# Optimization experiments

Measured on AMD Instinct MI355X. Metric: run time of the kernel, lower is better.

Reference implementation:

```python
import jax, jax.numpy as jnp
import numpy as np

B, N, C = 4, 2048, 1024
H = 8
D = C // H  # head dim = 128
SCALE = D ** -0.5
EPS = 1e-5


def setup_inputs() -> dict:
    key = jax.random.key(0)
    ks = jax.random.split(key, 12)
    s = 0.02
    return {
        "x": jax.random.normal(ks[0], (B, N, C), jnp.float32),
        "ln1_g": jnp.ones((C,), jnp.float32),
        "ln1_b": jnp.zeros((C,), jnp.float32),
        "w_qkv": jax.random.normal(ks[1], (3 * C, C), jnp.float32) * s,  # torch Linear weight [out,in], no bias
        "w_proj": jax.random.normal(ks[2], (C, C), jnp.float32) * s,
        "b_proj": jnp.zeros((C,), jnp.float32),
        "ln2_g": jnp.ones((C,), jnp.float32),
        "ln2_b": jnp.zeros((C,), jnp.float32),
        "w1": jax.random.normal(ks[3], (C, C), jnp.float32) * s,
        "b1": jnp.full((C,), 0.1, jnp.float32),
        "w2": jax.random.normal(ks[4], (C, C), jnp.float32) * s,
        "b2": jnp.full((C,), 0.1, jnp.float32),
        "bn_g": jnp.ones((C,), jnp.float32),
        "bn_b": jnp.zeros((C,), jnp.float32),
        "bn_mean": jnp.zeros((C,), jnp.float32),
        "bn_var": jnp.ones((C,), jnp.float32),
    }


def _layernorm(x, g, b):
    mu = jnp.mean(x, axis=-1, keepdims=True)
    var = jnp.mean(jnp.square(x - mu), axis=-1, keepdims=True)
    return (x - mu) * jax.lax.rsqrt(var + EPS) * g + b


def reference(x, ln1_g, ln1_b, w_qkv, w_proj, b_proj, ln2_g, ln2_b,
              w1, b1, w2, b2, bn_g, bn_b, bn_mean, bn_var):
    # --- attention branch (pre-LN) ---
    h = _layernorm(x, ln1_g, ln1_b)
    qkv = h @ w_qkv.T                              # [B,N,3C]
    qkv = qkv.reshape(B, N, 3, H, D)
    q = qkv[:, :, 0].transpose(0, 2, 1, 3)         # [B,H,N,D]
    k = qkv[:, :, 1].transpose(0, 2, 1, 3)
    v = qkv[:, :, 2].transpose(0, 2, 1, 3)
    attn = jnp.einsum('bhnd,bhmd->bhnm', q, k) * SCALE
    attn = jax.nn.softmax(attn, axis=-1)
    o = jnp.einsum('bhnm,bhmd->bhnd', attn, v)     # [B,H,N,D]
    o = o.transpose(0, 2, 1, 3).reshape(B, N, C)
    x = x + (o @ w_proj.T + b_proj)

    # --- MLP branch (pre-LN), ELU + eval-mode BatchNorm ---
    h = _layernorm(x, ln2_g, ln2_b)
    h = jax.nn.elu(h @ w1.T + b1)
    h = jax.nn.elu(h @ w2.T + b2)
    h = (h - bn_mean) * jax.lax.rsqrt(bn_var + EPS) * bn_g + bn_b
    return x + h
```

## Files before the change

kernel.cpp:

```cpp
#include <hip/hip_runtime.h>
#include <hip/hip_bf16.h>

using u16 = unsigned short;
typedef __attribute__((ext_vector_type(8))) __bf16 bf16x8;
typedef __attribute__((ext_vector_type(4))) float f32x4;
typedef __attribute__((ext_vector_type(16))) float f32x16;
typedef __attribute__((ext_vector_type(4))) unsigned int u32x4;

#define LN_EPS 1e-5f
#define ATT_SCALE 0.08838834764831845f

__device__ __forceinline__ u16 f2bf(float f) {
    unsigned int u = __builtin_bit_cast(unsigned int, f);
    u += 0x7FFFu + ((u >> 16) & 1u);
    return (u16)(u >> 16);
}

__device__ __forceinline__ bf16x8 ld_frag(const u16* p) {
    return __builtin_bit_cast(bf16x8, *(const u32x4*)p);
}

__device__ __forceinline__ unsigned pack_bf2(float lo, float hi) {
    return __builtin_amdgcn_perm(__builtin_bit_cast(unsigned, hi),
                                 __builtin_bit_cast(unsigned, lo), 0x07060302u);
}

__global__ void cvt_f32_bf16(const float* __restrict__ in, u16* __restrict__ out, int n4) {
    int i = blockIdx.x * blockDim.x + threadIdx.x;
    if (i < n4) {
        const float4 v = ((const float4*)in)[i];
        ushort4 o;
        o.x = f2bf(v.x); o.y = f2bf(v.y); o.z = f2bf(v.z); o.w = f2bf(v.w);
        ((ushort4*)out)[i] = o;
    }
}

__global__ __launch_bounds__(256)
void ln_kernel(const float* __restrict__ x, const float* __restrict__ g,
               const float* __restrict__ b, u16* __restrict__ out)
{
    const int row = blockIdx.x;
    const int t = threadIdx.x;
    const float4 v = ((const float4*)(x + (size_t)row * 1024))[t];
    float s  = v.x + v.y + v.z + v.w;
    float ss = v.x * v.x + v.y * v.y + v.z * v.z + v.w * v.w;
    #pragma unroll
    for (int d = 32; d > 0; d >>= 1) { s += __shfl_down(s, d); ss += __shfl_down(ss, d); }
    __shared__ float red[8];
    const int wave = t >> 6, lane = t & 63;
    if (lane == 0) { red[wave] = s; red[4 + wave] = ss; }
    __syncthreads();
    const float S  = red[0] + red[1] + red[2] + red[3];
    const float SS = red[4] + red[5] + red[6] + red[7];
    const float mu = S * (1.f / 1024.f);
    const float rstd = rsqrtf(SS * (1.f / 1024.f) - mu * mu + LN_EPS);
    const float4 gv = ((const float4*)g)[t];
    const float4 bv = ((const float4*)b)[t];
    ushort4 ov;
    ov.x = f2bf((v.x - mu) * rstd * gv.x + bv.x);
    ov.y = f2bf((v.y - mu) * rstd * gv.y + bv.y);
    ov.z = f2bf((v.z - mu) * rstd * gv.z + bv.z);
    ov.w = f2bf((v.w - mu) * rstd * gv.w + bv.w);
    ((ushort4*)(out + (size_t)row * 1024))[t] = ov;
}

template <int EPI>
__global__ __launch_bounds__(256, 2)
void gemm_bt(const u16* __restrict__ A, const u16* __restrict__ Bw,
             int M, int N, int K,
             const float* __restrict__ bias, const float* __restrict__ res,
             float* __restrict__ Cf, u16* __restrict__ Cb, u16* __restrict__ Cv,
             const float* __restrict__ bng, const float* __restrict__ bnb,
             const float* __restrict__ bnm, const float* __restrict__ bnv)
{
    __shared__ __align__(16) u16 As[128 * 32];
    __shared__ __align__(16) u16 Bs[128 * 32];

    const int tid  = threadIdx.x;
    const int wave = tid >> 6;
    const int lane = tid & 63;
    const int quad = lane >> 4;
    const int l16  = lane & 15;
    const int m0 = blockIdx.x * 128;
    const int n0 = blockIdx.y * 128;
    const int wm = (wave & 1) * 64;
    const int wn = (wave >> 1) * 64;

    f32x4 acc[4][4];
    #pragma unroll
    for (int i = 0; i < 4; i++)
        #pragma unroll
        for (int j = 0; j < 4; j++)
            acc[i][j] = f32x4{0.f, 0.f, 0.f, 0.f};

    const int srow = lane >> 2;
    const int scol = (lane & 3) * 8;
    const u16* gA0 = A  + (size_t)(m0 + wave * 32 + srow) * K + scol;
    const u16* gA1 = gA0 + (size_t)16 * K;
    const u16* gB0 = Bw + (size_t)(n0 + wave * 32 + srow) * K + scol;
    const u16* gB1 = gB0 + (size_t)16 * K;
    u16* lA0 = &As[(wave * 32) * 32];
    u16* lA1 = &As[(wave * 32 + 16) * 32];
    u16* lB0 = &Bs[(wave * 32) * 32];
    u16* lB1 = &Bs[(wave * 32 + 16) * 32];

    for (int k0 = 0; k0 < K; k0 += 32) {
        __builtin_amdgcn_global_load_lds((const __attribute__((address_space(1))) void*)(gA0 + k0),
                                         (__attribute__((address_space(3))) void*)lA0, 16, 0, 0);
        __builtin_amdgcn_global_load_lds((const __attribute__((address_space(1))) void*)(gA1 + k0),
                                         (__attribute__((address_space(3))) void*)lA1, 16, 0, 0);
        __builtin_amdgcn_global_load_lds((const __attribute__((address_space(1))) void*)(gB0 + k0),
                                         (__attribute__((address_space(3))) void*)lB0, 16, 0, 0);
        __builtin_amdgcn_global_load_lds((const __attribute__((address_space(1))) void*)(gB1 + k0),
                                         (__attribute__((address_space(3))) void*)lB1, 16, 0, 0);
        __syncthreads();
        bf16x8 af[4], bfv[4];
        #pragma unroll
        for (int i = 0; i < 4; i++) af[i]  = ld_frag(&As[(wm + i * 16 + l16) * 32 + quad * 8]);
        #pragma unroll
        for (int j = 0; j < 4; j++) bfv[j] = ld_frag(&Bs[(wn + j * 16 + l16) * 32 + quad * 8]);
        #pragma unroll
        for (int i = 0; i < 4; i++)
            #pragma unroll
            for (int j = 0; j < 4; j++)
                acc[i][j] = __builtin_amdgcn_mfma_f32_16x16x32_bf16(af[i], bfv[j], acc[i][j], 0, 0, 0);
        __syncthreads();
    }

    #pragma unroll
    for (int j = 0; j < 4; j++) {
        const int gn = n0 + wn + j * 16 + l16;
        float bs = 0.f, sc = 0.f, sh = 0.f;
        if constexpr (EPI >= 1) bs = bias[gn];
        if constexpr (EPI == 3) {
            const float iv = rsqrtf(bnv[gn] + LN_EPS);
            sc = bng[gn] * iv;
            sh = bnb[gn] - bnm[gn] * sc;
        }
        if constexpr (EPI == 0) {
            if (gn < 2048) {
                const float qs = (gn < 1024) ? ATT_SCALE : 1.0f;
                #pragma unroll
                for (int i = 0; i < 4; i++) {
                    const int gm0 = m0 + wm + i * 16 + quad * 4;
                    #pragma unroll
                    for (int r = 0; r < 4; r++)
                        Cb[(size_t)(gm0 + r) * 2048 + gn] = f2bf(acc[i][j][r] * qs);
                }
            } else {
                const int hh = (gn >> 7) & 7, dd = gn & 127;
                #pragma unroll
                for (int i = 0; i < 4; i++) {
                    const int gm0 = m0 + wm + i * 16 + quad * 4;
                    #pragma unroll
                    for (int r = 0; r < 4; r++) {
                        const int tok = gm0 + r;
                        Cv[((size_t)((tok >> 11) * 8 + hh) * 128 + dd) * 2048 + (tok & 2047)] =
                            f2bf(acc[i][j][r]);
                    }
                }
            }
        } else {
            #pragma unroll
            for (int i = 0; i < 4; i++) {
                const int gm0 = m0 + wm + i * 16 + quad * 4;
                #pragma unroll
                for (int r = 0; r < 4; r++) {
                    const size_t idx = (size_t)(gm0 + r) * N + gn;
                    const float v = acc[i][j][r];
                    if constexpr (EPI == 1) {
                        Cf[idx] = res[idx] + v + bs;
                    } else if constexpr (EPI == 2) {
                        float t = v + bs;
                        t = t > 0.f ? t : (__expf(t) - 1.f);
                        Cb[idx] = f2bf(t);
                    } else {
                        float t = v + bs;
                        t = t > 0.f ? t : (__expf(t) - 1.f);
                        t = t * sc + sh;
                        Cf[idx] = res[idx] + t;
                    }
                }
            }
        }
    }
}

__global__ __launch_bounds__(256, 2)
void attn_kernel(const u16* __restrict__ qk, const u16* __restrict__ vT, u16* __restrict__ o)
{
    __shared__ __align__(16) u16 smem[17408];

    const int tid  = threadIdx.x;
    const int wave = tid >> 6;
    const int lane = tid & 63;
    const int l32  = lane & 31;
    const int hl   = lane >> 5;
    const int qt   = blockIdx.x;
    const int bh   = blockIdx.y;
    const int b    = bh >> 3, h = bh & 7;
    const size_t tok0 = (size_t)b * 2048;

    const u16* qptr = qk + h * 128;
    const u16* kptr = qk + 1024 + h * 128;
    const u16* vptr = vT + (size_t)bh * 128 * 2048;

    #pragma unroll
    for (int qq = 0; qq < 8; qq++) {
        const int s = qq * 256 + tid;
        const int r = s >> 4;
        const int cg = (s & 15) ^ (r & 7);
        const u16* g = qptr + (tok0 + qt * 128 + r) * 2048 + cg * 8;
        const int sb = (qq * 256 + (tid & 192)) * 8;
        __builtin_amdgcn_global_load_lds((const __attribute__((address_space(1))) void*)g,
                                         (__attribute__((address_space(3))) void*)(smem + sb), 16, 0, 0);
    }
    __syncthreads();

    bf16x8 qf[8];
    {
        const int row = wave * 32 + l32;
        #pragma unroll
        for (int ks = 0; ks < 8; ks++) {
            const int c = (ks * 2 + hl) ^ (row & 7);
            qf[ks] = ld_frag(smem + row * 128 + c * 8);
        }
    }

    f32x16 oacc[4];
    #pragma unroll
    for (int i = 0; i < 4; i++)
        #pragma unroll
        for (int e = 0; e < 16; e++) oacc[i][e] = 0.f;
    float l_acc = 0.f;

    u16* Ks = smem;
    u16* Vs = smem + 8192;

    for (int kt = 0; kt < 32; kt++) {
        __syncthreads();
        #pragma unroll
        for (int qq = 0; qq < 4; qq++) {
            const int s = qq * 256 + tid;
            const int r = s >> 4;
            const int cg = (s & 15) ^ (r & 7);
            const u16* g = kptr + (tok0 + kt * 64 + r) * 2048 + cg * 8;
            const int sb = (qq * 256 + (tid & 192)) * 8;
            __builtin_amdgcn_global_load_lds((const __attribute__((address_space(1))) void*)g,
                                             (__attribute__((address_space(3))) void*)(Ks + sb), 16, 0, 0);
        }
        #pragma unroll
        for (int qq = 0; qq < 4; qq++) {
            const int s = qq * 256 + tid;
            const int r = s >> 3;
            const int cg = (s & 7) ^ (r & 7);
            const u16* g = vptr + (size_t)r * 2048 + kt * 64 + cg * 8;
            const int sb = (qq * 256 + (tid & 192)) * 8;
            __builtin_amdgcn_global_load_lds((const __attribute__((address_space(1))) void*)g,
                                             (__attribute__((address_space(3))) void*)(Vs + sb), 16, 0, 0);
        }
        __syncthreads();

        f32x16 sacc[2];
        #pragma unroll
        for (int t = 0; t < 2; t++)
            #pragma unroll
            for (int e = 0; e < 16; e++) sacc[t][e] = 0.f;
        #pragma unroll
        for (int ks = 0; ks < 8; ks++) {
            #pragma unroll
            for (int mt = 0; mt < 2; mt++) {
                const int row = mt * 32 + l32;
                const int c = (ks * 2 + hl) ^ (row & 7);
                const bf16x8 kf = ld_frag(Ks + row * 128 + c * 8);
                sacc[mt] = __builtin_amdgcn_mfma_f32_32x32x16_bf16(kf, qf[ks], sacc[mt], 0, 0, 0);
            }
        }

        unsigned pk[2][8];
        #pragma unroll
        for (int t = 0; t < 2; t++) {
            #pragma unroll
            for (int r2 = 0; r2 < 8; r2++) {
                const float p0 = __expf(sacc[t][2 * r2]);
                const float p1 = __expf(sacc[t][2 * r2 + 1]);
                l_acc += p0 + p1;
                pk[t][r2] = pack_bf2(p0, p1);
            }
        }

        #pragma unroll
        for (int ks = 0; ks < 4; ks++) {
            const int t = ks >> 1;
            const int pb = (ks & 1) * 4;
            const unsigned s0 = (unsigned)__shfl_xor((int)pk[t][pb + 0], 32);
            const unsigned s1 = (unsigned)__shfl_xor((int)pk[t][pb + 1], 32);
            const unsigned s2 = (unsigned)__shfl_xor((int)pk[t][pb + 2], 32);
            const unsigned s3 = (unsigned)__shfl_xor((int)pk[t][pb + 3], 32);
            u32x4 pu;
            pu.x = hl ? s2 : pk[t][pb + 0];
            pu.y = hl ? s3 : pk[t][pb + 1];
            pu.z = hl ? pk[t][pb + 2] : s0;
            pu.w = hl ? pk[t][pb + 3] : s1;
            const bf16x8 pf = __builtin_bit_cast(bf16x8, pu);
            #pragma unroll
            for (int dt = 0; dt < 4; dt++) {
                const int row = dt * 32 + l32;
                const int c = (ks * 2 + hl) ^ (row & 7);
                const bf16x8 vf = ld_frag(Vs + row * 64 + c * 8);
                oacc[dt] = __builtin_amdgcn_mfma_f32_32x32x16_bf16(vf, pf, oacc[dt], 0, 0, 0);
            }
        }
    }

    __syncthreads();
    u16* Ot = smem;
    const float lt  = l_acc + __shfl_xor(l_acc, 32);
    const float inv = 1.0f / lt;
    const int qloc = wave * 32 + l32;
    #pragma unroll
    for (int dt = 0; dt < 4; dt++) {
        #pragma unroll
        for (int r2 = 0; r2 < 8; r2++) {
            const float v0 = oacc[dt][2 * r2] * inv;
            const float v1 = oacc[dt][2 * r2 + 1] * inv;
            const int dp = dt * 32 + 4 * hl + 2 * (r2 & 1) + 8 * (r2 >> 1);
            *(unsigned*)(Ot + qloc * 136 + dp) = pack_bf2(v0, v1);
        }
    }
    __syncthreads();
    const int qr = tid >> 1;
    const int hh = tid & 1;
    const u16* src = Ot + qr * 136 + hh * 64;
    u16* dst = o + (tok0 + qt * 128 + qr) * 1024 + h * 128 + hh * 64;
    #pragma unroll
    for (int c = 0; c < 8; c++)
        *(u32x4*)(dst + c * 8) = *(const u32x4*)(src + c * 8);
}

extern "C" void kernel_launch(void* const* d_in, const int* in_sizes, int n_in,
                              void* d_out, int out_size, void* d_ws, size_t ws_size,
                              hipStream_t stream)
{
    const float* x      = (const float*)d_in[0];
    const float* ln1_g  = (const float*)d_in[1];
    const float* ln1_b  = (const float*)d_in[2];
    const float* w_qkv  = (const float*)d_in[3];
    const float* w_proj = (const float*)d_in[4];
    const float* b_proj = (const float*)d_in[5];
    const float* ln2_g  = (const float*)d_in[6];
    const float* ln2_b  = (const float*)d_in[7];
    const float* w1     = (const float*)d_in[8];
    const float* b1     = (const float*)d_in[9];
    const float* w2     = (const float*)d_in[10];
    const float* b2     = (const float*)d_in[11];
    const float* bn_g   = (const float*)d_in[12];
    const float* bn_b   = (const float*)d_in[13];
    const float* bn_m   = (const float*)d_in[14];
    const float* bn_v   = (const float*)d_in[15];
    float* out = (float*)d_out;

    u16* wq   = (u16*)d_ws;
    u16* wp   = wq  + (size_t)3072 * 1024;
    u16* w1b  = wp  + (size_t)1024 * 1024;
    u16* w2b  = w1b + (size_t)1024 * 1024;
    u16* hbuf = w2b + (size_t)1024 * 1024;
    u16* qkb  = hbuf + (size_t)8192 * 1024;
    u16* vTb  = qkb + (size_t)8192 * 2048;
    u16* obuf = vTb + (size_t)8192 * 1024;
    float* x1 = (float*)(obuf + (size_t)8192 * 1024);

    cvt_f32_bf16<<<3072, 256, 0, stream>>>(w_qkv,  wq,  3072 * 1024 / 4);
    cvt_f32_bf16<<<1024, 256, 0, stream>>>(w_proj, wp,  1024 * 1024 / 4);
    cvt_f32_bf16<<<1024, 256, 0, stream>>>(w1,     w1b, 1024 * 1024 / 4);
    cvt_f32_bf16<<<1024, 256, 0, stream>>>(w2,     w2b, 1024 * 1024 / 4);

    ln_kernel<<<8192, 256, 0, stream>>>(x, ln1_g, ln1_b, hbuf);

    gemm_bt<0><<<dim3(64, 24), 256, 0, stream>>>(hbuf, wq, 8192, 3072, 1024,
        nullptr, nullptr, nullptr, qkb, vTb, nullptr, nullptr, nullptr, nullptr);

    attn_kernel<<<dim3(16, 32), 256, 0, stream>>>(qkb, vTb, obuf);

    gemm_bt<1><<<dim3(64, 8), 256, 0, stream>>>(obuf, wp, 8192, 1024, 1024,
        b_proj, x, x1, nullptr, nullptr, nullptr, nullptr, nullptr, nullptr);

    ln_kernel<<<8192, 256, 0, stream>>>(x1, ln2_g, ln2_b, hbuf);

    gemm_bt<2><<<dim3(64, 8), 256, 0, stream>>>(hbuf, w1b, 8192, 1024, 1024,
        b1, nullptr, nullptr, obuf, nullptr, nullptr, nullptr, nullptr, nullptr);

    gemm_bt<3><<<dim3(64, 8), 256, 0, stream>>>(obuf, w2b, 8192, 1024, 1024,
        b2, x1, out, nullptr, nullptr, bn_g, bn_b, bn_m, bn_v);
}
```

Measured before the change: 396.2 us.

## Double-buffer K/V tiles in attention, remap blocks, and use smaller GEMM tiles for C-wide GEMMs

The attention kernel now double-buffers its K/V tiles in shared memory, prefetching the next tile while the current one is computed, and drops one barrier per iteration. Blocks are remapped with a 1D grid so that neighbouring blocks share heads, which should help L2 reuse. The three 1024-wide GEMMs move to a new 64x128 tile kernel with a higher occupancy hint, which doubles the block count for better CU fill. In exchange, attention uses more LDS (64KB), which may reduce occupancy, and the smaller GEMM tiles reuse each loaded tile less.

Measured after the change: 400.4 us. About the same (+1.1%).

```diff
diff --git a/kernel.cpp b/kernel.cpp
--- a/kernel.cpp
+++ b/kernel.cpp
@@ -23,6 +23,11 @@
 __device__ __forceinline__ unsigned pack_bf2(float lo, float hi) {
     return __builtin_amdgcn_perm(__builtin_bit_cast(unsigned, hi),
                                  __builtin_bit_cast(unsigned, lo), 0x07060302u);
+}
+
+__device__ __forceinline__ void gl_lds(const u16* g, u16* l) {
+    __builtin_amdgcn_global_load_lds((const __attribute__((address_space(1))) void*)g,
+                                     (__attribute__((address_space(3))) void*)l, 16, 0, 0);
 }
 
 __global__ void cvt_f32_bf16(const float* __restrict__ in, u16* __restrict__ out, int n4) {
@@ -64,15 +69,11 @@
     ((ushort4*)(out + (size_t)row * 1024))[t] = ov;
 }
 
-template <int EPI>
 __global__ __launch_bounds__(256, 2)
-void gemm_bt(const u16* __restrict__ A, const u16* __restrict__ Bw,
-             int M, int N, int K,
-             const float* __restrict__ bias, const float* __restrict__ res,
-             float* __restrict__ Cf, u16* __restrict__ Cb, u16* __restrict__ Cv,
-             const float* __restrict__ bng, const float* __restrict__ bnb,
-             const float* __restrict__ bnm, const float* __restrict__ bnv)
+void gemm_qkv(const u16* __restrict__ A, const u16* __restrict__ Bw,
+              u16* __restrict__ Cb, u16* __restrict__ Cv)
 {
+    const int M = 8192, N = 3072, K = 1024;
     __shared__ __align__(16) u16 As[128 * 32];
     __shared__ __align__(16) u16 Bs[128 * 32];
 
@@ -105,14 +106,10 @@
     u16* lB1 = &Bs[(wave * 32 + 16) * 32];
 
     for (int k0 = 0; k0 < K; k0 += 32) {
-        __builtin_amdgcn_global_load_lds((const __attribute__((address_space(1))) void*)(gA0 + k0),
-                                         (__attribute__((address_space(3))) void*)lA0, 16, 0, 0);
-        __builtin_amdgcn_global_load_lds((const __attribute__((address_space(1))) void*)(gA1 + k0),
-                                         (__attribute__((address_space(3))) void*)lA1, 16, 0, 0);
-        __builtin_amdgcn_global_load_lds((const __attribute__((address_space(1))) void*)(gB0 + k0),
-                                         (__attribute__((address_space(3))) void*)lB0, 16, 0, 0);
-        __builtin_amdgcn_global_load_lds((const __attribute__((address_space(1))) void*)(gB1 + k0),
-                                         (__attribute__((address_space(3))) void*)lB1, 16, 0, 0);
+        gl_lds(gA0 + k0, lA0);
+        gl_lds(gA1 + k0, lA1);
+        gl_lds(gB0 + k0, lB0);
+        gl_lds(gB1 + k0, lB1);
         __syncthreads();
         bf16x8 af[4], bfv[4];
         #pragma unroll
@@ -130,56 +127,114 @@
     #pragma unroll
     for (int j = 0; j < 4; j++) {
         const int gn = n0 + wn + j * 16 + l16;
-        float bs = 0.f, sc = 0.f, sh = 0.f;
-        if constexpr (EPI >= 1) bs = bias[gn];
+        if (gn < 2048) {
+            const float qs = (gn < 1024) ? ATT_SCALE : 1.0f;
+            #pragma unroll
+            for (int i = 0; i < 4; i++) {
+                const int gm0 = m0 + wm + i * 16 + quad * 4;
+                #pragma unroll
+                for (int r = 0; r < 4; r++)
+                    Cb[(size_t)(gm0 + r) * 2048 + gn] = f2bf(acc[i][j][r] * qs);
+            }
+        } else {
+            const int hh = (gn >> 7) & 7, dd = gn & 127;
+            #pragma unroll
+            for (int i = 0; i < 4; i++) {
+                const int gm0 = m0 + wm + i * 16 + quad * 4;
+                #pragma unroll
+                for (int r = 0; r < 4; r++) {
+                    const int tok = gm0 + r;
+                    Cv[((size_t)((tok >> 11) * 8 + hh) * 128 + dd) * 2048 + (tok & 2047)] =
+                        f2bf(acc[i][j][r]);
+                }
+            }
+        }
+    }
+}
+
+template <int EPI>
+__global__ __launch_bounds__(256, 4)
+void gemm_c(const u16* __restrict__ A, const u16* __restrict__ Bw,
+            const float* __restrict__ bias, const float* __restrict__ res,
+            float* __restrict__ Cf, u16* __restrict__ Cb,
+            const float* __restrict__ bng, const float* __restrict__ bnb,
+            const float* __restrict__ bnm, const float* __restrict__ bnv)
+{
+    const int N = 1024, K = 1024;
+    __shared__ __align__(16) u16 As[64 * 32];
+    __shared__ __align__(16) u16 Bs[128 * 32];
+
+    const int tid  = threadIdx.x;
+    const int wave = tid >> 6;
+    const int lane = tid & 63;
+    const int quad = lane >> 4;
+    const int l16  = lane & 15;
+    const int m0 = blockIdx.x * 64;
+    const int n0 = blockIdx.y * 128;
+    const int wm = (wave & 1) * 32;
+    const int wn = (wave >> 1) * 64;
+
+    f32x4 acc[2][4];
+    #pragma unroll
+    for (int i = 0; i < 2; i++)
+        #pragma unroll
+        for (int j = 0; j < 4; j++)
+            acc[i][j] = f32x4{0.f, 0.f, 0.f, 0.f};
+
+    const int srow = tid >> 2;
+    const int scol = (tid & 3) * 8;
+    const u16* gA  = A  + (size_t)(m0 + srow) * K + scol;
+    const u16* gB0 = Bw + (size_t)(n0 + srow) * K + scol;
+    const u16* gB1 = gB0 + (size_t)64 * K;
+    u16* lA  = &As[wave * 512];
+    u16* lB0 = &Bs[wave * 512];
+    u16* lB1 = &Bs[2048 + wave * 512];
+
+    for (int k0 = 0; k0 < K; k0 += 32) {
+        gl_lds(gA  + k0, lA);
+        gl_lds(gB0 + k0, lB0);
+        gl_lds(gB1 + k0, lB1);
+        __syncthreads();
+        bf16x8 af[2], bfv[4];
+        #pragma unroll
+        for (int i = 0; i < 2; i++) af[i]  = ld_frag(&As[(wm + i * 16 + l16) * 32 + quad * 8]);
+        #pragma unroll
+        for (int j = 0; j < 4; j++) bfv[j] = ld_frag(&Bs[(wn + j * 16 + l16) * 32 + quad * 8]);
+        #pragma unroll
+        for (int i = 0; i < 2; i++)
+            #pragma unroll
+            for (int j = 0; j < 4; j++)
+                acc[i][j] = __builtin_amdgcn_mfma_f32_16x16x32_bf16(af[i], bfv[j], acc[i][j], 0, 0, 0);
+        __syncthreads();
+    }
+
+    #pragma unroll
+    for (int j = 0; j < 4; j++) {
+        const int gn = n0 + wn + j * 16 + l16;
+        float bs = bias[gn], sc = 0.f, sh = 0.f;
         if constexpr (EPI == 3) {
             const float iv = rsqrtf(bnv[gn] + LN_EPS);
             sc = bng[gn] * iv;
             sh = bnb[gn] - bnm[gn] * sc;
         }
-        if constexpr (EPI == 0) {
-            if (gn < 2048) {
-                const float qs = (gn < 1024) ? ATT_SCALE : 1.0f;
-                #pragma unroll
-                for (int i = 0; i < 4; i++) {
-                    const int gm0 = m0 + wm + i * 16 + quad * 4;
-                    #pragma unroll
-                    for (int r = 0; r < 4; r++)
-                        Cb[(size_t)(gm0 + r) * 2048 + gn] = f2bf(acc[i][j][r] * qs);
-                }
-            } else {
-                const int hh = (gn >> 7) & 7, dd = gn & 127;
-                #pragma unroll
-                for (int i = 0; i < 4; i++) {
-                    const int gm0 = m0 + wm + i * 16 + quad * 4;
-                    #pragma unroll
-                    for (int r = 0; r < 4; r++) {
-                        const int tok = gm0 + r;
-                        Cv[((size_t)((tok >> 11) * 8 + hh) * 128 + dd) * 2048 + (tok & 2047)] =
-                            f2bf(acc[i][j][r]);
-                    }
-                }
-            }
-        } else {
-            #pragma unroll
-            for (int i = 0; i < 4; i++) {
-                const int gm0 = m0 + wm + i * 16 + quad * 4;
-                #pragma unroll
-                for (int r = 0; r < 4; r++) {
-                    const size_t idx = (size_t)(gm0 + r) * N + gn;
-                    const float v = acc[i][j][r];
-                    if constexpr (EPI == 1) {
-                        Cf[idx] = res[idx] + v + bs;
-                    } else if constexpr (EPI == 2) {
-                        float t = v + bs;
-                        t = t > 0.f ? t : (__expf(t) - 1.f);
-                        Cb[idx] = f2bf(t);
-                    } else {
-                        float t = v + bs;
-                        t = t > 0.f ? t : (__expf(t) - 1.f);
-                        t = t * sc + sh;
-                        Cf[idx] = res[idx] + t;
-                    }
+        #pragma unroll
+        for (int i = 0; i < 2; i++) {
+            const int gm0 = m0 + wm + i * 16 + quad * 4;
+            #pragma unroll
+            for (int r = 0; r < 4; r++) {
+                const size_t idx = (size_t)(gm0 + r) * N + gn;
+                const float v = acc[i][j][r];
+                if constexpr (EPI == 1) {
+                    Cf[idx] = res[idx] + v + bs;
+                } else if constexpr (EPI == 2) {
+                    float t = v + bs;
+                    t = t > 0.f ? t : (__expf(t) - 1.f);
+                    Cb[idx] = f2bf(t);
+                } else {
+                    float t = v + bs;
+                    t = t > 0.f ? t : (__expf(t) - 1.f);
+                    t = t * sc + sh;
+                    Cf[idx] = res[idx] + t;
                 }
             }
         }
@@ -189,15 +244,16 @@
 __global__ __launch_bounds__(256, 2)
 void attn_kernel(const u16* __restrict__ qk, const u16* __restrict__ vT, u16* __restrict__ o)
 {
-    __shared__ __align__(16) u16 smem[17408];
+    __shared__ __align__(16) u16 smem[32768];
 
     const int tid  = threadIdx.x;
     const int wave = tid >> 6;
     const int lane = tid & 63;
     const int l32  = lane & 31;
     const int hl   = lane >> 5;
-    const int qt   = blockIdx.x;
-    const int bh   = blockIdx.y;
+    const int id   = blockIdx.x;
+    const int bh   = ((id >> 7) << 3) | (id & 7);
+    const int qt   = (id >> 3) & 15;
     const int b    = bh >> 3, h = bh & 7;
     const size_t tok0 = (size_t)b * 2048;
 
@@ -211,9 +267,8 @@
         const int r = s >> 4;
         const int cg = (s & 15) ^ (r & 7);
         const u16* g = qptr + (tok0 + qt * 128 + r) * 2048 + cg * 8;
-        const int sb = (qq * 256 + (tid & 192)) * 8;
-        __builtin_amdgcn_global_load_lds((const __attribute__((address_space(1))) void*)g,
-                                         (__attribute__((address_space(3))) void*)(smem + sb), 16, 0, 0);
+        const int sb = 16384 + (qq * 256 + (tid & 192)) * 8;
+        gl_lds(g, smem + sb);
     }
     __syncthreads();
 
@@ -223,7 +278,7 @@
         #pragma unroll
         for (int ks = 0; ks < 8; ks++) {
             const int c = (ks * 2 + hl) ^ (row & 7);
-            qf[ks] = ld_frag(smem + row * 128 + c * 8);
+            qf[ks] = ld_frag(smem + 16384 + row * 128 + c * 8);
         }
     }
 
@@ -234,32 +289,38 @@
         for (int e = 0; e < 16; e++) oacc[i][e] = 0.f;
     float l_acc = 0.f;
 
-    u16* Ks = smem;
-    u16* Vs = smem + 8192;
+    {
+        #pragma unroll
+        for (int qq = 0; qq < 4; qq++) {
+            const int s = qq * 256 + tid;
+            const int rk = s >> 4, ck = (s & 15) ^ (rk & 7);
+            gl_lds(kptr + (tok0 + rk) * 2048 + ck * 8,
+                   smem + (qq * 256 + (tid & 192)) * 8);
+            const int rv = s >> 3, cv = (s & 7) ^ (rv & 7);
+            gl_lds(vptr + (size_t)rv * 2048 + cv * 8,
+                   smem + 8192 + (qq * 256 + (tid & 192)) * 8);
+        }
+    }
 
     for (int kt = 0; kt < 32; kt++) {
         __syncthreads();
-        #pragma unroll
-        for (int qq = 0; qq < 4; qq++) {
-            const int s = qq * 256 + tid;
-            const int r = s >> 4;
-            const int cg = (s & 15) ^ (r & 7);
-            const u16* g = kptr + (tok0 + kt * 64 + r) * 2048 + cg * 8;
-            const int sb = (qq * 256 + (tid & 192)) * 8;
-            __builtin_amdgcn_global_load_lds((const __attribute__((address_space(1))) void*)g,
-                                             (__attribute__((address_space(3))) void*)(Ks + sb), 16, 0, 0);
-        }
-        #pragma unroll
-        for (int qq = 0; qq < 4; qq++) {
-            const int s = qq * 256 + tid;
-            const int r = s >> 3;
-            const int cg = (s & 7) ^ (r & 7);
-            const u16* g = vptr + (size_t)r * 2048 + kt * 64 + cg * 8;
-            const int sb = (qq * 256 + (tid & 192)) * 8;
-            __builtin_amdgcn_global_load_lds((const __attribute__((address_space(1))) void*)g,
-                                             (__attribute__((address_space(3))) void*)(Vs + sb), 16, 0, 0);
-        }
-        __syncthreads();
+
+        if (kt + 1 < 32) {
+            u16* nb = smem + ((kt + 1) & 1) * 16384;
+            #pragma unroll
+            for (int qq = 0; qq < 4; qq++) {
+                const int s = qq * 256 + tid;
+                const int rk = s >> 4, ck = (s & 15) ^ (rk & 7);
+                gl_lds(kptr + (tok0 + (kt + 1) * 64 + rk) * 2048 + ck * 8,
+                       nb + (qq * 256 + (tid & 192)) * 8);
+                const int rv = s >> 3, cv = (s & 7) ^ (rv & 7);
+                gl_lds(vptr + (size_t)rv * 2048 + (kt + 1) * 64 + cv * 8,
+                       nb + 8192 + (qq * 256 + (tid & 192)) * 8);
+            }
+        }
+
+        const u16* Ks = smem + (kt & 1) * 16384;
+        const u16* Vs = Ks + 8192;
 
         f32x16 sacc[2];
         #pragma unroll
@@ -377,19 +438,18 @@
 
     ln_kernel<<<8192, 256, 0, stream>>>(x, ln1_g, ln1_b, hbuf);
 
-    gemm_bt<0><<<dim3(64, 24), 256, 0, stream>>>(hbuf, wq, 8192, 3072, 1024,
-        nullptr, nullptr, nullptr, qkb, vTb, nullptr, nullptr, nullptr, nullptr);
-
-    attn_kernel<<<dim3(16, 32), 256, 0, stream>>>(qkb, vTb, obuf);
-
-    gemm_bt<1><<<dim3(64, 8), 256, 0, stream>>>(obuf, wp, 8192, 1024, 1024,
-        b_proj, x, x1, nullptr, nullptr, nullptr, nullptr, nullptr, nullptr);
+    gemm_qkv<<<dim3(64, 24), 256, 0, stream>>>(hbuf, wq, qkb, vTb);
+
+    attn_kernel<<<512, 256, 0, stream>>>(qkb, vTb, obuf);
+
+    gemm_c<1><<<dim3(128, 8), 256, 0, stream>>>(obuf, wp,
+        b_proj, x, x1, nullptr, nullptr, nullptr, nullptr, nullptr);
 
     ln_kernel<<<8192, 256, 0, stream>>>(x1, ln2_g, ln2_b, hbuf);
 
-    gemm_bt<2><<<dim3(64, 8), 256, 0, stream>>>(hbuf, w1b, 8192, 1024, 1024,
-        b1, nullptr, nullptr, obuf, nullptr, nullptr, nullptr, nullptr, nullptr);
-
-    gemm_bt<3><<<dim3(64, 8), 256, 0, stream>>>(obuf, w2b, 8192, 1024, 1024,
-        b2, x1, out, nullptr, nullptr, bn_g, bn_b, bn_m, bn_v);
-}
+    gemm_c<2><<<dim3(128, 8), 256, 0, stream>>>(hbuf, w1b,
+        b1, nullptr, nullptr, obuf, nullptr, nullptr, nullptr, nullptr);
+
+    gemm_c<3><<<dim3(128, 8), 256, 0, stream>>>(obuf, w2b,
+        b2, x1, out, nullptr, bn_g, bn_b, bn_m, bn_v);
+}
```
